# Kernel tuning notes

Measured on AMD Instinct MI355X. Metric: run time of the kernel, lower is better.

The kernel has to match this reference:

```python
import jax, jax.numpy as jnp
import numpy as np

NEG_SLOPE = 0.2  # PyG GATConv default leaky_relu slope


def gat_conv(x_src, x_dst, src, dst, Ws, Wd, a_s, a_d, bias, n_dst, heads, ch,
             concat, edge_w=None, We=None, a_e=None):
    """PyG-style GATConv (bipartite, add_self_loops=False, eval mode)."""
    hs = (x_src @ Ws).reshape(-1, heads, ch)   # [Ns,H,C]
    hd = (x_dst @ Wd).reshape(-1, heads, ch)   # [Nd,H,C]
    a_src = jnp.einsum('nhc,hc->nh', hs, a_s)  # [Ns,H]
    a_dst = jnp.einsum('nhc,hc->nh', hd, a_d)  # [Nd,H]
    logits = a_src[src] + a_dst[dst]           # [E,H]
    if edge_w is not None:
        he = (edge_w[:, None] @ We).reshape(-1, heads, ch)  # lin_edge proj
        logits = logits + jnp.einsum('ehc,hc->eh', he, a_e)
    logits = jax.nn.leaky_relu(logits, NEG_SLOPE)
    # segment softmax grouped by destination node
    m = jax.ops.segment_max(logits, dst, num_segments=n_dst)
    e = jnp.exp(logits - m[dst])
    denom = jax.ops.segment_sum(e, dst, num_segments=n_dst)
    alpha = e / denom[dst]                     # [E,H]
    out = jax.ops.segment_sum(hs[src] * alpha[..., None], dst, num_segments=n_dst)
    out = out.reshape(n_dst, heads * ch) if concat else out.mean(axis=1)
    return out + bias


def setup_inputs() -> dict:
    key = jax.random.key(0)
    ks = jax.random.split(key, 40)
    NA = NB = 50000
    F = 128
    E = 800000
    HID = 100
    d = {}
    d['x_A'] = jax.random.normal(ks[0], (NA, F), jnp.float32)
    d['x_B'] = jax.random.normal(ks[1], (NB, F), jnp.float32)
    d['ei_AB'] = jax.random.randint(ks[2], (2, E), 0, NA)  # row0=src in A, row1=dst in B
    d['ei_BA'] = jax.random.randint(ks[3], (2, E), 0, NB)
    d['w_AB'] = jax.random.uniform(ks[4], (E,), jnp.float32)
    d['w_BA'] = jax.random.uniform(ks[5], (E,), jnp.float32)
    idx = [6]
    def p(shape):
        v = jax.random.normal(ks[idx[0]], shape, jnp.float32) * 0.1
        idx[0] += 1
        return v
    for et in ('AB', 'BA'):
        d['l1_%s_Ws' % et] = p((F, HID)); d['l1_%s_Wd' % et] = p((F, HID))
        d['l1_%s_as' % et] = p((4, 25)); d['l1_%s_ad' % et] = p((4, 25))
        d['l1_%s_We' % et] = p((1, HID)); d['l1_%s_ae' % et] = p((4, 25))
        d['l1_%s_b' % et] = p((HID,))
        d['l2_%s_Ws' % et] = p((HID, HID)); d['l2_%s_Wd' % et] = p((HID, HID))
        d['l2_%s_as' % et] = p((1, HID)); d['l2_%s_ad' % et] = p((1, HID))
        d['l2_%s_b' % et] = p((HID,))
    return d


def reference(x_A, x_B, ei_AB, ei_BA, w_AB, w_BA,
              l1_AB_Ws, l1_AB_Wd, l1_AB_as, l1_AB_ad, l1_AB_We, l1_AB_ae, l1_AB_b,
              l1_BA_Ws, l1_BA_Wd, l1_BA_as, l1_BA_ad, l1_BA_We, l1_BA_ae, l1_BA_b,
              l2_AB_Ws, l2_AB_Wd, l2_AB_as, l2_AB_ad, l2_AB_b,
              l2_BA_Ws, l2_BA_Wd, l2_BA_as, l2_BA_ad, l2_BA_b):
    NA, NB = x_A.shape[0], x_B.shape[0]
    s_ab, d_ab = ei_AB[0], ei_AB[1]
    s_ba, d_ba = ei_BA[0], ei_BA[1]
    # layer 1: heads=4, out=25 per head, concat -> 100, edge_dim=1
    hB = gat_conv(x_A, x_B, s_ab, d_ab, l1_AB_Ws, l1_AB_Wd, l1_AB_as, l1_AB_ad,
                  l1_AB_b, NB, 4, 25, True, w_AB, l1_AB_We, l1_AB_ae)
    hA = gat_conv(x_B, x_A, s_ba, d_ba, l1_BA_Ws, l1_BA_Wd, l1_BA_as, l1_BA_ad,
                  l1_BA_b, NA, 4, 25, True, w_BA, l1_BA_We, l1_BA_ae)
    # dropout is identity in eval mode
    hA = jax.nn.elu(hA)
    hB = jax.nn.elu(hB)
    # layer 2: heads=1, out=100, concat=False (mean over 1 head), no edge_dim
    oB = gat_conv(hA, hB, s_ab, d_ab, l2_AB_Ws, l2_AB_Wd, l2_AB_as, l2_AB_ad,
                  l2_AB_b, NB, 1, 100, False)
    oA = gat_conv(hB, hA, s_ba, d_ba, l2_BA_Ws, l2_BA_Wd, l2_BA_as, l2_BA_ad,
                  l2_BA_b, NA, 1, 100, False)
    return jnp.stack([oA, oB])  # [2, 50000, 100]
```

## Files before the change

kernel.cpp:

```cpp
#include <hip/hip_runtime.h>


#define NNODES 50000
#define NEDGES 800000
#define SCAN_T 1024
#define SCAN_NBLK ((NNODES + SCAN_T - 1) / SCAN_T)

typedef unsigned short u16;
typedef unsigned int u32;

__device__ __forceinline__ float b2f(u16 u) {
    union { u32 i; float f; } x;
    x.i = ((u32)u) << 16;
    return x.f;
}
__device__ __forceinline__ u16 f2b(float f) {
    union { float f; u32 i; } x;
    x.f = f;
    u32 r = x.i + 0x7FFFu + ((x.i >> 16) & 1u);
    return (u16)(r >> 16);
}

__global__ void ce_kernel(const float* __restrict__ WeA, const float* __restrict__ aeA,
                          const float* __restrict__ WeB, const float* __restrict__ aeB,
                          float* __restrict__ ce ) {
    const float* We = blockIdx.x ? WeB : WeA;
    const float* ae = blockIdx.x ? aeB : aeA;
    __shared__ float s[4];
    int tid = threadIdx.x;
    if (tid < 4) s[tid] = 0.f;
    __syncthreads();
    if (tid < 100) atomicAdd(&s[tid / 25], We[tid] * ae[tid]);
    __syncthreads();
    if (tid < 4) ce[blockIdx.x * 4 + tid] = s[tid];
}

__global__ void count_kernel(const int* __restrict__ eiA, const int* __restrict__ eiB,
                             int E, int* cntA, int* cntB) {
    int i = blockIdx.x * blockDim.x + threadIdx.x;
    if (i < E) atomicAdd(&cntA[eiA[E + i]], 1);
    else if (i < 2 * E) atomicAdd(&cntB[eiB[E + (i - E)]], 1);
}

__global__ __launch_bounds__(SCAN_T) void scanA_kernel(
    const int* __restrict__ cntA, const int* __restrict__ cntB,
    int* __restrict__ roA, int* __restrict__ roB, int* __restrict__ partial, int N) {
    const int dir = blockIdx.y;
    const int* cnt = dir ? cntB : cntA;
    int* ro = dir ? roB : roA;
    const int tid = threadIdx.x;
    const int i = blockIdx.x * SCAN_T + tid;
    __shared__ int sm[SCAN_T];
    sm[tid] = (i < N) ? cnt[i] : 0;
    __syncthreads();
    for (int off = 1; off < SCAN_T; off <<= 1) {
        int t = (tid >= off) ? sm[tid - off] : 0;
        __syncthreads();
        sm[tid] += t;
        __syncthreads();
    }
    if (i < N) ro[i + 1] = sm[tid];
    if (tid == SCAN_T - 1) partial[dir * 64 + blockIdx.x] = sm[tid];
}

__global__ void scanB_kernel(int* __restrict__ partial, int nblk) {
    __shared__ int sm[128];
    const int tid = threadIdx.x;
    sm[tid] = ((tid & 63) < nblk) ? partial[tid] : 0;
    __syncthreads();
    if (tid < 2) {
        int run = 0;
        for (int b = 0; b < nblk; ++b) {
            int t = sm[tid * 64 + b];
            sm[tid * 64 + b] = run;
            run += t;
        }
    }
    __syncthreads();
    partial[tid] = sm[tid];
}

__global__ __launch_bounds__(SCAN_T) void scanC_kernel(
    const int* __restrict__ cntA, const int* __restrict__ cntB,
    int* __restrict__ roA, int* __restrict__ roB,
    int* __restrict__ curA, int* __restrict__ curB,
    const int* __restrict__ partial, int N) {
    const int dir = blockIdx.y;
    const int* cnt = dir ? cntB : cntA;
    int* ro = dir ? roB : roA;
    int* cur = dir ? curB : curA;
    const int poff = partial[dir * 64 + blockIdx.x];
    const int i = blockIdx.x * SCAN_T + threadIdx.x;
    if (i < N) {
        int c = cnt[i];
        int r = ro[i + 1] + poff;
        ro[i + 1] = r;
        cur[i] = r - c;
        if (i == 0) ro[0] = 0;
    }
}

__global__ void fill_kernel(const int* __restrict__ eiA, const int* __restrict__ eiB,
                            const float* __restrict__ wA, const float* __restrict__ wB,
                            int E, int* curA, int* curB,
                            int* __restrict__ ssA, int* __restrict__ ssB,
                            int* __restrict__ sdA, int* __restrict__ sdB,
                            float* __restrict__ swA, float* __restrict__ swB) {
    int i = blockIdx.x * blockDim.x + threadIdx.x;
    if (i < E) {
        int s = eiA[i], d = eiA[E + i];
        int pos = atomicAdd(&curA[d], 1);
        ssA[pos] = s; sdA[pos] = d; swA[pos] = wA[i];
    } else if (i < 2 * E) {
        int j = i - E;
        int s = eiB[j], d = eiB[E + j];
        int pos = atomicAdd(&curB[d], 1);
        ssB[pos] = s; sdB[pos] = d; swB[pos] = wB[j];
    }
}

struct GemmArgs {
    const float* X;
    const float* W;
    const float* a;
    void* H;
    float* att;
};

template <int K, int HEADS>
__global__ __launch_bounds__(256, 2) void gemm_att_kernel(
    GemmArgs g0, GemmArgs g1, GemmArgs g2, GemmArgs g3, int N) {
    const GemmArgs ga[4] = {g0, g1, g2, g3};
    const GemmArgs g = ga[blockIdx.y];
    constexpr int XS_STRIDE = 33;
    constexpr int XS_BUF = 128 * XS_STRIDE;
    constexpr int WS_STRIDE = 28;
    constexpr int WS_WAVE = 32 * WS_STRIDE;
    constexpr int WS_BUF = 4 * WS_WAVE;
    constexpr int SMEM_BYTES = (2 * XS_BUF + 2 * WS_BUF) * 4;
    __shared__ __align__(16) char smem[SMEM_BYTES];
    const int tid = threadIdx.x;
    const int lane = tid & 63;
    const int w = tid >> 6;
    const int node0 = blockIdx.x * 128;
    const int nA = node0 + lane;
    const int nB = node0 + 64 + lane;
    const bool vA = nA < N, vB = nB < N;

    const int c0 = __builtin_amdgcn_readfirstlane(25 * w);

    float acc0[25], acc1[25];
#pragma unroll
    for (int j = 0; j < 25; ++j) { acc0[j] = 0.f; acc1[j] = 0.f; }

    float* Xs = (float*)smem;
    float* Wsh = (float*)smem + 2 * XS_BUF;
    float4 rv[4];
    float wv[13];

    auto issue_x = [&](int k0) {
#pragma unroll
        for (int r = 0; r < 4; ++r) {
            const int s = tid + r * 256;
            const int n = s >> 3;
            const int ko = (s & 7) * 4;
            int row = node0 + n;
            if (row >= N) row = N - 1;
            const float* xp = g.X + (size_t)row * K + k0 + ko;
            if constexpr (K % 32 == 0) {
                rv[r] = *(const float4*)xp;
            } else {
                const int kb = k0 + ko;
                float4 v = make_float4(0.f, 0.f, 0.f, 0.f);
                if (kb + 3 < K) {
                    v = *(const float4*)xp;
                } else {
                    if (kb < K) v.x = xp[0];
                    if (kb + 1 < K) v.y = xp[1];
                    if (kb + 2 < K) v.z = xp[2];
                }
                rv[r] = v;
            }
        }
    };
    auto write_x = [&](int buf) {
#pragma unroll
        for (int r = 0; r < 4; ++r) {
            const int s = tid + r * 256;
            const int n = s >> 3;
            const int ko = (s & 7) * 4;
            float* dst = Xs + buf * XS_BUF + n * XS_STRIDE + ko;
            dst[0] = rv[r].x;
            dst[1] = rv[r].y;
            dst[2] = rv[r].z;
            dst[3] = rv[r].w;
        }
    };
    auto issue_w = [&](int k0, int kc) {
        const int lim = kc * 100;
#pragma unroll
        for (int r = 0; r < 13; ++r) {
            const int e = tid + r * 256;
            wv[r] = (e < lim) ? g.W[(size_t)k0 * 100 + e] : 0.f;
        }
    };
    auto write_w = [&](int buf, int kc) {
        const int lim = kc * 100;
#pragma unroll
        for (int r = 0; r < 13; ++r) {
            const int e = tid + r * 256;
            if (e < lim) {
                const int k = e / 100;
                const int j = e - k * 100;
                const int hd = j / 25;
                const int jj = j - hd * 25;
                Wsh[buf * WS_BUF + hd * WS_WAVE + k * WS_STRIDE + jj] = wv[r];
            }
        }
    };

    constexpr int C = (K + 31) / 32;
    {
        const int kc0 = (K < 32) ? K : 32;
        issue_x(0);
        issue_w(0, kc0);
        write_x(0);
        write_w(0, kc0);
    }
    __syncthreads();
    for (int c = 0; c < C; ++c) {
        const int k0 = c * 32;
        const int kc = (K - k0 < 32) ? (K - k0) : 32;
        const int kcn = (K - k0 - 32 < 32) ? (K - k0 - 32) : 32;
        if (c + 1 < C) {
            issue_x(k0 + 32);
            issue_w(k0 + 32, kcn);
        }
        const float* x0p = Xs + (c & 1) * XS_BUF + lane * XS_STRIDE;
        const float* x1p = x0p + 64 * XS_STRIDE;
        const float* wp = Wsh + (c & 1) * WS_BUF + w * WS_WAVE;
#pragma unroll 4
        for (int kk = 0; kk < kc; ++kk) {
            const float xs0 = x0p[kk];
            const float xs1 = x1p[kk];
            float wr[25];
#pragma unroll
            for (int j = 0; j < 25; ++j) wr[j] = wp[kk * WS_STRIDE + j];
#pragma unroll
            for (int j = 0; j < 25; ++j) {
                acc0[j] = fmaf(xs0, wr[j], acc0[j]);
                acc1[j] = fmaf(xs1, wr[j], acc1[j]);
            }
        }
        if (c + 1 < C) {
            __syncthreads();
            write_x((c + 1) & 1);
            write_w((c + 1) & 1, kcn);
        }
        __syncthreads();
    }

    float ap0 = 0.f, ap1 = 0.f;
#pragma unroll
    for (int j = 0; j < 25; ++j) {
        const float av = g.a[c0 + j];
        ap0 = fmaf(acc0[j], av, ap0);
        ap1 = fmaf(acc1[j], av, ap1);
    }

    const int rem = N - node0;
    if (HEADS == 4) {
        if (g.att != nullptr) {
            const float w0 = (g.H != nullptr) ? b2f(f2b(ap0)) : ap0;
            const float w1 = (g.H != nullptr) ? b2f(f2b(ap1)) : ap1;
            if (vA) g.att[(size_t)nA * 4 + w] = w0;
            if (vB) g.att[(size_t)nB * 4 + w] = w1;
        }
        if (g.H != nullptr) {
            u16* sh = (u16*)smem;
            u32* sh32 = (u32*)smem;
#pragma unroll
            for (int j = 0; j < 25; ++j) sh[lane * 106 + c0 + j] = f2b(acc0[j]);
            sh[lane * 106 + 100 + w] = f2b(ap0);
            __syncthreads();
            {
                const int limA = ((rem < 64) ? rem : 64) * 52;
                u32* Hb = (u32*)g.H + (size_t)node0 * 64;
                for (int i = tid; i < 64 * 52; i += 256) {
                    if (i < limA) {
                        int nd = i / 52;
                        int off = i - nd * 52;
                        Hb[nd * 64 + off] = sh32[nd * 53 + off];
                    }
                }
            }
            __syncthreads();
#pragma unroll
            for (int j = 0; j < 25; ++j) sh[lane * 106 + c0 + j] = f2b(acc1[j]);
            sh[lane * 106 + 100 + w] = f2b(ap1);
            __syncthreads();
            {
                const int remB = rem - 64;
                const int limB = ((remB < 64) ? (remB < 0 ? 0 : remB) : 64) * 52;
                u32* Hb = (u32*)g.H + (size_t)(node0 + 64) * 64;
                for (int i = tid; i < 64 * 52; i += 256) {
                    if (i < limB) {
                        int nd = i / 52;
                        int off = i - nd * 52;
                        Hb[nd * 64 + off] = sh32[nd * 53 + off];
                    }
                }
            }
        }
    } else {
        u16* sh = (u16*)smem;
        u32* sh32 = (u32*)smem;
        float* attp = (float*)(smem + 64 * 102 * 2);
        attp[w * 128 + lane] = ap0;
        attp[w * 128 + 64 + lane] = ap1;
        if (g.H != nullptr) {
#pragma unroll
            for (int j = 0; j < 25; ++j) sh[lane * 102 + c0 + j] = f2b(acc0[j]);
            __syncthreads();
            {
                const int limA = ((rem < 64) ? rem : 64) * 50;
                u32* Hb = (u32*)g.H + (size_t)node0 * 64;
                for (int i = tid; i < 64 * 50; i += 256) {
                    if (i < limA) {
                        int nd = i / 50;
                        int off = i - nd * 50;
                        Hb[nd * 64 + off] = sh32[nd * 51 + off];
                    }
                }
                if (tid < 128 && node0 + tid < N)
                    g.att[node0 + tid] =
                        attp[tid] + attp[128 + tid] + attp[256 + tid] + attp[384 + tid];
            }
            __syncthreads();
#pragma unroll
            for (int j = 0; j < 25; ++j) sh[lane * 102 + c0 + j] = f2b(acc1[j]);
            __syncthreads();
            {
                const int remB = rem - 64;
                const int limB = ((remB < 64) ? (remB < 0 ? 0 : remB) : 64) * 50;
                u32* Hb = (u32*)g.H + (size_t)(node0 + 64) * 64;
                for (int i = tid; i < 64 * 50; i += 256) {
                    if (i < limB) {
                        int nd = i / 50;
                        int off = i - nd * 50;
                        Hb[nd * 64 + off] = sh32[nd * 51 + off];
                    }
                }
            }
        } else {
            __syncthreads();
            if (tid < 128 && node0 + tid < N)
                g.att[node0 + tid] =
                    attp[tid] + attp[128 + tid] + attp[256 + tid] + attp[384 + tid];
        }
    }
}

struct EdgeP4Args {
    const int* ss;
    const int* sd;
    const float* sw;
    const float* aS;
    const float* aD;
    const float* ce;
    float* p4;
};

__global__ void edge_p4_kernel(EdgeP4Args a0, EdgeP4Args a1, int E) {
    const EdgeP4Args a = blockIdx.y ? a1 : a0;
    const int e = blockIdx.x * 256 + threadIdx.x;
    if (e >= E) return;
    const int s = a.ss[e];
    const int d = a.sd[e];
    const float w = a.sw[e];
    const float4 as4 = *(const float4*)(a.aS + (size_t)s * 4);
    const float4 ad4 = *(const float4*)(a.aD + (size_t)d * 4);
    float4 p;
    float l;
    l = as4.x + ad4.x + w * a.ce[0]; l = fmaxf(l, 0.2f * l); p.x = __expf(l);
    l = as4.y + ad4.y + w * a.ce[1]; l = fmaxf(l, 0.2f * l); p.y = __expf(l);
    l = as4.z + ad4.z + w * a.ce[2]; l = fmaxf(l, 0.2f * l); p.z = __expf(l);
    l = as4.w + ad4.w + w * a.ce[3]; l = fmaxf(l, 0.2f * l); p.w = __expf(l);
    *(float4*)(a.p4 + (size_t)e * 4) = p;
}

struct EdgeP1Args {
    const int* ss;
    const int* sd;
    const float* aS;
    const float* aD;
    float* p1;
};

__global__ void edge_p1_kernel(EdgeP1Args a0, EdgeP1Args a1, int E) {
    const EdgeP1Args a = blockIdx.y ? a1 : a0;
    const int e = blockIdx.x * 256 + threadIdx.x;
    if (e >= E) return;
    const int s = a.ss[e];
    const int d = a.sd[e];
    float l = a.aS[s] + a.aD[d];
    l = fmaxf(l, 0.2f * l);
    a.p1[e] = __expf(l);
}

struct Gather4Args {
    const int* ro;
    const int* ss;
    const u16* hp;
    const float* p4;
    const float* bias;
    float* outp;
};

__global__ __launch_bounds__(256) void gather4_kernel(Gather4Args ga0, Gather4Args ga1, int Nd) {
    const Gather4Args ga[2] = {ga0, ga1};
    const Gather4Args g = ga[blockIdx.y];
    int wid = (int)((blockIdx.x * blockDim.x + threadIdx.x) >> 6);
    if (wid >= Nd) return;
    const int n = __builtin_amdgcn_readfirstlane(wid);
    const int lane = threadIdx.x & 63;
    const int beg = g.ro[n], end = g.ro[n + 1];
    const bool act = (lane < 50);
    const int cc0 = act ? 2 * lane : 0;
    const int h0 = cc0 / 25;
    const int h1 = (cc0 + 1) / 25;
    const int aoff = 2 * (h0 >> 1);
    float acc0 = 0.f, acc1 = 0.f, d0 = 0.f, d1 = 0.f;

    auto edge = [&](u32 va, float2 pp, float& p0o, float& p1o) {
        const float p0 = (h0 & 1) ? pp.y : pp.x;
        const float p1 = (h1 & 1) ? pp.y : pp.x;
        acc0 = fmaf(p0, b2f((u16)va), acc0);
        acc1 = fmaf(p1, b2f((u16)(va >> 16)), acc1);
        p0o = p0;
        p1o = p1;
    };

    struct G4 { u32 va0, va1, va2, va3; float2 pp0, pp1, pp2, pp3; };
    auto load4 = [&](int off) -> G4 {
        G4 r;
        const int o = __builtin_amdgcn_readfirstlane(off);
        const int s0 = g.ss[o];
        const int s1 = g.ss[o + 1];
        const int s2 = g.ss[o + 2];
        const int s3 = g.ss[o + 3];
        r.pp0 = *(const float2*)(g.p4 + (size_t)o * 4 + aoff);
        r.pp1 = *(const float2*)(g.p4 + (size_t)(o + 1) * 4 + aoff);
        r.pp2 = *(const float2*)(g.p4 + (size_t)(o + 2) * 4 + aoff);
        r.pp3 = *(const float2*)(g.p4 + (size_t)(o + 3) * 4 + aoff);
        r.va0 = *(const u32*)(g.hp + (size_t)s0 * 128 + cc0);
        r.va1 = *(const u32*)(g.hp + (size_t)s1 * 128 + cc0);
        r.va2 = *(const u32*)(g.hp + (size_t)s2 * 128 + cc0);
        r.va3 = *(const u32*)(g.hp + (size_t)s3 * 128 + cc0);
        return r;
    };
    auto compute4 = [&](const G4& e) {
        float pa0, pa1, pb0, pb1;
        edge(e.va0, e.pp0, pa0, pa1);
        edge(e.va1, e.pp1, pb0, pb1);
        d0 += pa0 + pb0;
        d1 += pa1 + pb1;
        edge(e.va2, e.pp2, pa0, pa1);
        edge(e.va3, e.pp3, pb0, pb1);
        d0 += pa0 + pb0;
        d1 += pa1 + pb1;
    };

    int i = beg;
    const int last4 = beg + ((end - beg) & ~3);
    const int ng = (last4 - beg) >> 2;
    if (ng >= 2) {
        G4 cur = load4(i);
        G4 nxt = load4(i + 4);
        i += 8;
        for (; i < last4; i += 4) {
            G4 nn = load4(i);
            __builtin_amdgcn_sched_barrier(0);
            compute4(cur);
            cur = nxt;
            nxt = nn;
        }
        compute4(cur);
        compute4(nxt);
    } else if (ng == 1) {
        G4 cur = load4(i);
        compute4(cur);
        i += 4;
    }
    if (i + 1 < end) {
        const int o = __builtin_amdgcn_readfirstlane(i);
        const int s0 = g.ss[o], s1 = g.ss[o + 1];
        const float2 pp0 = *(const float2*)(g.p4 + (size_t)o * 4 + aoff);
        const float2 pp1 = *(const float2*)(g.p4 + (size_t)(o + 1) * 4 + aoff);
        const u32 va0 = *(const u32*)(g.hp + (size_t)s0 * 128 + cc0);
        const u32 va1 = *(const u32*)(g.hp + (size_t)s1 * 128 + cc0);
        float pa0, pa1, pb0, pb1;
        edge(va0, pp0, pa0, pa1);
        edge(va1, pp1, pb0, pb1);
        d0 += pa0 + pb0;
        d1 += pa1 + pb1;
        i += 2;
    }
    if (i < end) {
        const int o = __builtin_amdgcn_readfirstlane(i);
        const int s0 = g.ss[o];
        const float2 pp0 = *(const float2*)(g.p4 + (size_t)o * 4 + aoff);
        const u32 va0 = *(const u32*)(g.hp + (size_t)s0 * 128 + cc0);
        float pa0, pa1;
        edge(va0, pp0, pa0, pa1);
        d0 += pa0;
        d1 += pa1;
    }

    if (act) {
        float r0 = (end > beg) ? acc0 / d0 : 0.f;
        float r1 = (end > beg) ? acc1 / d1 : 0.f;
        r0 += g.bias[cc0];
        r0 = (r0 > 0.f) ? r0 : (__expf(r0) - 1.f);
        r1 += g.bias[cc0 + 1];
        r1 = (r1 > 0.f) ? r1 : (__expf(r1) - 1.f);
        *(float2*)(g.outp + (size_t)n * 100 + cc0) = make_float2(r0, r1);
    }
}

struct Gather1Args {
    const int* ro;
    const int* ss;
    const u16* hp;
    const float* p1;
    const float* bias;
    float* outp;
};

__global__ __launch_bounds__(256) void gather1_kernel(Gather1Args ga0, Gather1Args ga1, int Nd) {
    const Gather1Args ga[2] = {ga0, ga1};
    const Gather1Args g = ga[blockIdx.y];
    int wid = (int)((blockIdx.x * blockDim.x + threadIdx.x) >> 6);
    if (wid >= Nd) return;
    const int n = __builtin_amdgcn_readfirstlane(wid);
    const int lane = threadIdx.x & 63;
    const int beg = g.ro[n], end = g.ro[n + 1];
    const bool act = (lane < 50);
    const int cc0 = act ? 2 * lane : 0;
    float acc0 = 0.f, acc1 = 0.f, d0 = 0.f;

    auto edge = [&](u32 va, float p) {
        acc0 = fmaf(p, b2f((u16)va), acc0);
        acc1 = fmaf(p, b2f((u16)(va >> 16)), acc1);
    };

    struct G1 { u32 va0, va1, va2, va3; float p0, p1, p2, p3; };
    auto load4 = [&](int off) -> G1 {
        G1 r;
        const int o = __builtin_amdgcn_readfirstlane(off);
        const int s0 = g.ss[o];
        const int s1 = g.ss[o + 1];
        const int s2 = g.ss[o + 2];
        const int s3 = g.ss[o + 3];
        r.p0 = g.p1[o];
        r.p1 = g.p1[o + 1];
        r.p2 = g.p1[o + 2];
        r.p3 = g.p1[o + 3];
        r.va0 = *(const u32*)(g.hp + (size_t)s0 * 128 + cc0);
        r.va1 = *(const u32*)(g.hp + (size_t)s1 * 128 + cc0);
        r.va2 = *(const u32*)(g.hp + (size_t)s2 * 128 + cc0);
        r.va3 = *(const u32*)(g.hp + (size_t)s3 * 128 + cc0);
        return r;
    };
    auto compute4 = [&](const G1& e) {
        edge(e.va0, e.p0);
        edge(e.va1, e.p1);
        d0 += e.p0 + e.p1;
        edge(e.va2, e.p2);
        edge(e.va3, e.p3);
        d0 += e.p2 + e.p3;
    };

    int i = beg;
    const int last4 = beg + ((end - beg) & ~3);
    const int ng = (last4 - beg) >> 2;
    if (ng >= 2) {
        G1 cur = load4(i);
        G1 nxt = load4(i + 4);
        i += 8;
        for (; i < last4; i += 4) {
            G1 nn = load4(i);
            __builtin_amdgcn_sched_barrier(0);
            compute4(cur);
            cur = nxt;
            nxt = nn;
        }
        compute4(cur);
        compute4(nxt);
    } else if (ng == 1) {
        G1 cur = load4(i);
        compute4(cur);
        i += 4;
    }
    if (i + 1 < end) {
        const int o = __builtin_amdgcn_readfirstlane(i);
        const int s0 = g.ss[o], s1 = g.ss[o + 1];
        const float p0 = g.p1[o], p1v = g.p1[o + 1];
        const u32 va0 = *(const u32*)(g.hp + (size_t)s0 * 128 + cc0);
        const u32 va1 = *(const u32*)(g.hp + (size_t)s1 * 128 + cc0);
        edge(va0, p0);
        edge(va1, p1v);
        d0 += p0 + p1v;
        i += 2;
    }
    if (i < end) {
        const int o = __builtin_amdgcn_readfirstlane(i);
        const int s0 = g.ss[o];
        const float p0 = g.p1[o];
        const u32 va0 = *(const u32*)(g.hp + (size_t)s0 * 128 + cc0);
        edge(va0, p0);
        d0 += p0;
    }

    if (act) {
        float r0 = (end > beg) ? acc0 / d0 : 0.f;
        float r1 = (end > beg) ? acc1 / d0 : 0.f;
        r0 += g.bias[cc0];
        r1 += g.bias[cc0 + 1];
        *(float2*)(g.outp + (size_t)n * 100 + cc0) = make_float2(r0, r1);
    }
}

extern "C" void kernel_launch(void* const* d_in, const int* in_sizes, int n_in,
                              void* d_out, int out_size, void* d_ws, size_t ws_size,
                              hipStream_t stream) {
    const float* x_A   = (const float*)d_in[0];
    const float* x_B   = (const float*)d_in[1];
    const int*   ei_AB = (const int*)d_in[2];
    const int*   ei_BA = (const int*)d_in[3];
    const float* w_AB  = (const float*)d_in[4];
    const float* w_BA  = (const float*)d_in[5];
    const float* l1AB_Ws = (const float*)d_in[6];
    const float* l1AB_Wd = (const float*)d_in[7];
    const float* l1AB_as = (const float*)d_in[8];
    const float* l1AB_ad = (const float*)d_in[9];
    const float* l1AB_We = (const float*)d_in[10];
    const float* l1AB_ae = (const float*)d_in[11];
    const float* l1AB_b  = (const float*)d_in[12];
    const float* l2AB_Ws = (const float*)d_in[13];
    const float* l2AB_Wd = (const float*)d_in[14];
    const float* l2AB_as = (const float*)d_in[15];
    const float* l2AB_ad = (const float*)d_in[16];
    const float* l2AB_b  = (const float*)d_in[17];
    const float* l1BA_Ws = (const float*)d_in[18];
    const float* l1BA_Wd = (const float*)d_in[19];
    const float* l1BA_as = (const float*)d_in[20];
    const float* l1BA_ad = (const float*)d_in[21];
    const float* l1BA_We = (const float*)d_in[22];
    const float* l1BA_ae = (const float*)d_in[23];
    const float* l1BA_b  = (const float*)d_in[24];
    const float* l2BA_Ws = (const float*)d_in[25];
    const float* l2BA_Wd = (const float*)d_in[26];
    const float* l2BA_as = (const float*)d_in[27];
    const float* l2BA_ad = (const float*)d_in[28];
    const float* l2BA_b  = (const float*)d_in[29];

    const int N = NNODES, E = NEDGES;

    size_t o = 0;
    auto alloc = [&](size_t n) { size_t r = o; o += (n + 63) & ~(size_t)63; return r; };
    size_t cntA = alloc(N), cntB = alloc(N);
    size_t roA = alloc(N + 1), roB = alloc(N + 1);
    size_t curA = alloc(N), curB = alloc(N);
    size_t ssA = alloc(E), ssB = alloc(E);
    size_t sdA = alloc(E), sdB = alloc(E);
    size_t swA = alloc(E), swB = alloc(E);
    size_t ce8 = alloc(8);
    size_t part = alloc(128);
    size_t pHAB = alloc((size_t)N * 64);
    size_t pHBA = alloc((size_t)N * 64);
    size_t ad1B = alloc((size_t)N * 4), ad1A = alloc((size_t)N * 4);
    size_t aS1AB = alloc((size_t)N * 4), aS1BA = alloc((size_t)N * 4);
    size_t p4AB = alloc((size_t)E * 4), p4BA = alloc((size_t)E * 4);
    size_t hA1 = alloc((size_t)N * 100), hB1 = alloc((size_t)N * 100);
    size_t H2AB = alloc((size_t)N * 64);
    size_t H2BA = alloc((size_t)N * 64);
    size_t as2AB = alloc(N), as2BA = alloc(N);
    size_t ad2AB = alloc(N), ad2BA = alloc(N);
    size_t p1AB = alloc(E), p1BA = alloc(E);
    (void)ws_size;

    float* wsf = (float*)d_ws;
    int*   wsi = (int*)d_ws;
    u32*   wsu = (u32*)d_ws;

    hipMemsetAsync(wsi + cntA, 0, sizeof(int) * (cntB + N - cntA), stream);

    ce_kernel<<<2, 128, 0, stream>>>(l1AB_We, l1AB_ae, l1BA_We, l1BA_ae, wsf + ce8);

    const int eb = (2 * E + 255) / 256;
    const int eb1 = (E + 255) / 256;
    count_kernel<<<eb, 256, 0, stream>>>(ei_AB, ei_BA, E, wsi + cntA, wsi + cntB);
    scanA_kernel<<<dim3(SCAN_NBLK, 2), SCAN_T, 0, stream>>>(
        wsi + cntA, wsi + cntB, wsi + roA, wsi + roB, wsi + part, N);
    scanB_kernel<<<1, 128, 0, stream>>>(wsi + part, SCAN_NBLK);
    scanC_kernel<<<dim3(SCAN_NBLK, 2), SCAN_T, 0, stream>>>(
        wsi + cntA, wsi + cntB, wsi + roA, wsi + roB, wsi + curA, wsi + curB, wsi + part, N);
    fill_kernel<<<eb, 256, 0, stream>>>(ei_AB, ei_BA, w_AB, w_BA, E, wsi + curA, wsi + curB,
                                        wsi + ssA, wsi + ssB, wsi + sdA, wsi + sdB,
                                        wsf + swA, wsf + swB);

    const int gb = (N + 127) / 128;
    {
        GemmArgs g0 = {x_A, l1AB_Ws, l1AB_as, (void*)(wsu + pHAB), wsf + aS1AB};
        GemmArgs g1 = {x_B, l1AB_Wd, l1AB_ad, nullptr, wsf + ad1B};
        GemmArgs g2 = {x_B, l1BA_Ws, l1BA_as, (void*)(wsu + pHBA), wsf + aS1BA};
        GemmArgs g3 = {x_A, l1BA_Wd, l1BA_ad, nullptr, wsf + ad1A};
        gemm_att_kernel<128, 4><<<dim3(gb, 4), 256, 0, stream>>>(g0, g1, g2, g3, N);
    }

    {
        EdgeP4Args a0 = {wsi + ssA, wsi + sdA, wsf + swA, wsf + aS1AB, wsf + ad1B,
                         wsf + ce8, wsf + p4AB};
        EdgeP4Args a1 = {wsi + ssB, wsi + sdB, wsf + swB, wsf + aS1BA, wsf + ad1A,
                         wsf + ce8 + 4, wsf + p4BA};
        edge_p4_kernel<<<dim3(eb1, 2), 256, 0, stream>>>(a0, a1, E);
    }

    const int wb = (N + 3) / 4;
    {
        Gather4Args g0 = {wsi + roA, wsi + ssA, (const u16*)(wsu + pHAB), wsf + p4AB,
                          l1AB_b, wsf + hB1};
        Gather4Args g1 = {wsi + roB, wsi + ssB, (const u16*)(wsu + pHBA), wsf + p4BA,
                          l1BA_b, wsf + hA1};
        gather4_kernel<<<dim3(wb, 2), 256, 0, stream>>>(g0, g1, N);
    }

    {
        GemmArgs g0 = {wsf + hA1, l2AB_Ws, l2AB_as, (void*)(wsu + H2AB), wsf + as2AB};
        GemmArgs g1 = {wsf + hB1, l2AB_Wd, l2AB_ad, nullptr, wsf + ad2AB};
        GemmArgs g2 = {wsf + hB1, l2BA_Ws, l2BA_as, (void*)(wsu + H2BA), wsf + as2BA};
        GemmArgs g3 = {wsf + hA1, l2BA_Wd, l2BA_ad, nullptr, wsf + ad2BA};
        gemm_att_kernel<100, 1><<<dim3(gb, 4), 256, 0, stream>>>(g0, g1, g2, g3, N);
    }

    {
        EdgeP1Args a0 = {wsi + ssA, wsi + sdA, wsf + as2AB, wsf + ad2AB, wsf + p1AB};
        EdgeP1Args a1 = {wsi + ssB, wsi + sdB, wsf + as2BA, wsf + ad2BA, wsf + p1BA};
        edge_p1_kernel<<<dim3(eb1, 2), 256, 0, stream>>>(a0, a1, E);
    }

    float* out = (float*)d_out;
    {
        Gather1Args g0 = {wsi + roA, wsi + ssA, (const u16*)(wsu + H2AB), wsf + p1AB,
                          l2AB_b, out + (size_t)N * 100};
        Gather1Args g1 = {wsi + roB, wsi + ssB, (const u16*)(wsu + H2BA), wsf + p1BA,
                          l2BA_b, out};
        gather1_kernel<<<dim3(wb, 2), 256, 0, stream>>>(g0, g1, N);
    }
}
```

Before: 928.0 us.

## Split each destination node's edge list across two wavefronts with LDS reduction

Both gather kernels now give each destination node two wavefronts instead of one. Each wavefront processes half of the node's CSR edge range, and the partial sums and denominators are combined through shared memory before the final normalize, bias and activation step. This doubles the independent memory-latency streams per node, which should help these latency-bound irregular gathers with about 16 edges per node. The cost is twice as many blocks, a __syncthreads per block, LDS traffic for the reduction, and half of the wavefronts sitting idle during the epilogue.

```diff
diff --git a/kernel.cpp b/kernel.cpp
--- a/kernel.cpp
+++ b/kernel.cpp
@@ -420,17 +420,26 @@
 __global__ __launch_bounds__(256) void gather4_kernel(Gather4Args ga0, Gather4Args ga1, int Nd) {
     const Gather4Args ga[2] = {ga0, ga1};
     const Gather4Args g = ga[blockIdx.y];
-    int wid = (int)((blockIdx.x * blockDim.x + threadIdx.x) >> 6);
-    if (wid >= Nd) return;
-    const int n = __builtin_amdgcn_readfirstlane(wid);
-    const int lane = threadIdx.x & 63;
-    const int beg = g.ro[n], end = g.ro[n + 1];
+    const int tid = threadIdx.x;
+    const int w = tid >> 6;
+    const int lane = tid & 63;
+    const int n = __builtin_amdgcn_readfirstlane((int)(blockIdx.x * 2 + (w >> 1)));
+    const int half = w & 1;
+    __shared__ float red[4][4][64];
+
     const bool act = (lane < 50);
     const int cc0 = act ? 2 * lane : 0;
     const int h0 = cc0 / 25;
     const int h1 = (cc0 + 1) / 25;
     const int aoff = 2 * (h0 >> 1);
     float acc0 = 0.f, acc1 = 0.f, d0 = 0.f, d1 = 0.f;
+
+    int nbeg = 0, nend = 0;
+    if (n < Nd) { nbeg = g.ro[n]; nend = g.ro[n + 1]; }
+    const int len = nend - nbeg;
+    const int hlen = (len + 1) >> 1;
+    const int beg = nbeg + (half ? hlen : 0);
+    const int end = half ? nend : (nbeg + hlen);
 
     auto edge = [&](u32 va, float2 pp, float& p0o, float& p1o) {
         const float p0 = (h0 & 1) ? pp.y : pp.x;
@@ -517,9 +526,18 @@
         d1 += pa1;
     }
 
-    if (act) {
-        float r0 = (end > beg) ? acc0 / d0 : 0.f;
-        float r1 = (end > beg) ? acc1 / d1 : 0.f;
+    red[w][0][lane] = acc0;
+    red[w][1][lane] = acc1;
+    red[w][2][lane] = d0;
+    red[w][3][lane] = d1;
+    __syncthreads();
+    if (half == 0 && n < Nd && act) {
+        acc0 += red[w + 1][0][lane];
+        acc1 += red[w + 1][1][lane];
+        d0   += red[w + 1][2][lane];
+        d1   += red[w + 1][3][lane];
+        float r0 = (len > 0) ? acc0 / d0 : 0.f;
+        float r1 = (len > 0) ? acc1 / d1 : 0.f;
         r0 += g.bias[cc0];
         r0 = (r0 > 0.f) ? r0 : (__expf(r0) - 1.f);
         r1 += g.bias[cc0 + 1];
@@ -540,14 +558,23 @@
 __global__ __launch_bounds__(256) void gather1_kernel(Gather1Args ga0, Gather1Args ga1, int Nd) {
     const Gather1Args ga[2] = {ga0, ga1};
     const Gather1Args g = ga[blockIdx.y];
-    int wid = (int)((blockIdx.x * blockDim.x + threadIdx.x) >> 6);
-    if (wid >= Nd) return;
-    const int n = __builtin_amdgcn_readfirstlane(wid);
-    const int lane = threadIdx.x & 63;
-    const int beg = g.ro[n], end = g.ro[n + 1];
+    const int tid = threadIdx.x;
+    const int w = tid >> 6;
+    const int lane = tid & 63;
+    const int n = __builtin_amdgcn_readfirstlane((int)(blockIdx.x * 2 + (w >> 1)));
+    const int half = w & 1;
+    __shared__ float red[4][3][64];
+
     const bool act = (lane < 50);
     const int cc0 = act ? 2 * lane : 0;
     float acc0 = 0.f, acc1 = 0.f, d0 = 0.f;
+
+    int nbeg = 0, nend = 0;
+    if (n < Nd) { nbeg = g.ro[n]; nend = g.ro[n + 1]; }
+    const int len = nend - nbeg;
+    const int hlen = (len + 1) >> 1;
+    const int beg = nbeg + (half ? hlen : 0);
+    const int end = half ? nend : (nbeg + hlen);
 
     auto edge = [&](u32 va, float p) {
         acc0 = fmaf(p, b2f((u16)va), acc0);
@@ -622,9 +649,16 @@
         d0 += p0;
     }
 
-    if (act) {
-        float r0 = (end > beg) ? acc0 / d0 : 0.f;
-        float r1 = (end > beg) ? acc1 / d0 : 0.f;
+    red[w][0][lane] = acc0;
+    red[w][1][lane] = acc1;
+    red[w][2][lane] = d0;
+    __syncthreads();
+    if (half == 0 && n < Nd && act) {
+        acc0 += red[w + 1][0][lane];
+        acc1 += red[w + 1][1][lane];
+        d0   += red[w + 1][2][lane];
+        float r0 = (len > 0) ? acc0 / d0 : 0.f;
+        float r1 = (len > 0) ? acc1 / d0 : 0.f;
         r0 += g.bias[cc0];
         r1 += g.bias[cc0 + 1];
         *(float2*)(g.outp + (size_t)n * 100 + cc0) = make_float2(r0, r1);
@@ -727,13 +761,13 @@
         edge_p4_kernel<<<dim3(eb1, 2), 256, 0, stream>>>(a0, a1, E);
     }
 
-    const int wb = (N + 3) / 4;
+    const int wb2 = (N + 1) / 2;
     {
         Gather4Args g0 = {wsi + roA, wsi + ssA, (const u16*)(wsu + pHAB), wsf + p4AB,
                           l1AB_b, wsf + hB1};
         Gather4Args g1 = {wsi + roB, wsi + ssB, (const u16*)(wsu + pHBA), wsf + p4BA,
                           l1BA_b, wsf + hA1};
-        gather4_kernel<<<dim3(wb, 2), 256, 0, stream>>>(g0, g1, N);
+        gather4_kernel<<<dim3(wb2, 2), 256, 0, stream>>>(g0, g1, N);
     }
 
     {
@@ -756,6 +790,6 @@
                           l2AB_b, out + (size_t)N * 100};
         Gather1Args g1 = {wsi + roB, wsi + ssB, (const u16*)(wsu + H2BA), wsf + p1BA,
                           l2BA_b, out};
-        gather1_kernel<<<dim3(wb, 2), 256, 0, stream>>>(g0, g1, N);
-    }
-}
+        gather1_kernel<<<dim3(wb2, 2), 256, 0, stream>>>(g0, g1, N);
+    }
+}
```

Result: slower. 1.112 ms (+19.8%).
